# Kernel optimization log

Measured on AMD Instinct MI355X. Metric: run time of the kernel, lower is better.

The kernel has to match this reference:

```python
import jax, jax.numpy as jnp
import numpy as np

BATCH = 32768
HIDDEN = 512
OUT = 2
FUTURE_STEPS = 60


def _lstm_cell(x, h, c, w_ih, w_hh, b_ih, b_hh):
    # PyTorch gate order: i, f, g, o
    g = x @ w_ih.T + h @ w_hh.T + b_ih + b_hh
    i, f, gg, o = jnp.split(g, 4, axis=-1)
    c_new = jax.nn.sigmoid(f) * c + jax.nn.sigmoid(i) * jnp.tanh(gg)
    h_new = jax.nn.sigmoid(o) * jnp.tanh(c_new)
    return h_new, c_new


def setup_inputs() -> dict:
    key = jax.random.key(0)
    ks = jax.random.split(key, 16)
    s = 0.05
    inp = {
        "h": jax.random.normal(ks[0], (BATCH, HIDDEN), jnp.float32),
        "w_init_h": jax.random.normal(ks[1], (HIDDEN, HIDDEN), jnp.float32) * s,
        "b_init_h": jax.random.normal(ks[2], (HIDDEN,), jnp.float32) * s,
        "w_init_c": jax.random.normal(ks[3], (HIDDEN, HIDDEN), jnp.float32) * s,
        "b_init_c": jax.random.normal(ks[4], (HIDDEN,), jnp.float32) * s,
        "w_ih0": jax.random.normal(ks[5], (4 * HIDDEN, OUT), jnp.float32) * s,
        "w_hh0": jax.random.normal(ks[6], (4 * HIDDEN, HIDDEN), jnp.float32) * s,
        "b_ih0": jax.random.normal(ks[7], (4 * HIDDEN,), jnp.float32) * s,
        "b_hh0": jax.random.normal(ks[8], (4 * HIDDEN,), jnp.float32) * s,
        "w_ih1": jax.random.normal(ks[9], (4 * HIDDEN, HIDDEN), jnp.float32) * s,
        "w_hh1": jax.random.normal(ks[10], (4 * HIDDEN, HIDDEN), jnp.float32) * s,
        "b_ih1": jax.random.normal(ks[11], (4 * HIDDEN,), jnp.float32) * s,
        "b_hh1": jax.random.normal(ks[12], (4 * HIDDEN,), jnp.float32) * s,
        "w_out": jax.random.normal(ks[13], (OUT, HIDDEN), jnp.float32) * s,
        "b_out": jax.random.normal(ks[14], (OUT,), jnp.float32) * s,
    }
    return inp


def reference(h, w_init_h, b_init_h, w_init_c, b_init_c,
              w_ih0, w_hh0, b_ih0, b_hh0,
              w_ih1, w_hh1, b_ih1, b_hh1,
              w_out, b_out):
    batch = h.shape[0]
    # same initial (h, c) replicated to both LSTM layers (repeat(2,1,1))
    h0 = h @ w_init_h.T + b_init_h
    c0 = h @ w_init_c.T + b_init_c
    x0 = jnp.zeros((batch, OUT), h.dtype)

    def step(carry, _):
        x, h1, c1, h2, c2 = carry
        h1, c1 = _lstm_cell(x, h1, c1, w_ih0, w_hh0, b_ih0, b_hh0)
        h2, c2 = _lstm_cell(h1, h2, c2, w_ih1, w_hh1, b_ih1, b_hh1)
        pred = h2 @ w_out.T + b_out  # [batch, OUT]
        return (pred, h1, c1, h2, c2), pred

    _, preds = jax.lax.scan(step, (x0, h0, c0, h0, c0), None, length=FUTURE_STEPS)
    return jnp.transpose(preds, (1, 0, 2))  # [batch, future_steps, OUT]
```

## Files before the change

kernel.cpp:

```cpp
#include <hip/hip_runtime.h>

#define HID    512
#define TPB    512
#define NSTEP  60
#define BMI    64

using f32x4 = __attribute__((ext_vector_type(4))) float;
using s16x8 = __attribute__((ext_vector_type(8))) short;

__device__ __forceinline__ unsigned short f2bf(float f) {
    unsigned u = __builtin_bit_cast(unsigned, f);
    u += 0x7fffu + ((u >> 16) & 1u);
    return (unsigned short)(u >> 16);
}
__device__ __forceinline__ float bf2f(unsigned u) {
    return __builtin_bit_cast(float, u << 16);
}
__device__ __forceinline__ float sigm(float x) { return 1.0f / (1.0f + __expf(-x)); }
__device__ __forceinline__ float tanh_(float x) { return 1.0f - 2.0f / (__expf(2.0f * x) + 1.0f); }

__device__ __forceinline__ f32x4 deperm(f32x4 q, int lgr) {
    f32x4 p;
    if (lgr == 0)      { p[0]=q[0]; p[1]=q[1]; p[2]=q[2]; p[3]=q[3]; }
    else if (lgr == 1) { p[0]=q[1]; p[1]=q[0]; p[2]=q[3]; p[3]=q[2]; }
    else if (lgr == 2) { p[0]=q[2]; p[1]=q[3]; p[2]=q[0]; p[3]=q[1]; }
    else               { p[0]=q[3]; p[1]=q[2]; p[2]=q[1]; p[3]=q[0]; }
    return p;
}

__global__ void pack_kernel(const float* __restrict__ w_hh0, const float* __restrict__ w_ih1,
                            const float* __restrict__ w_hh1, const float* __restrict__ w_init_h,
                            const float* __restrict__ w_init_c,
                            const float* __restrict__ b_ih0, const float* __restrict__ b_hh0,
                            const float* __restrict__ b_ih1, const float* __restrict__ b_hh1,
                            unsigned short* __restrict__ PW1, unsigned short* __restrict__ PW2,
                            unsigned short* __restrict__ PI,
                            float* __restrict__ b1, float* __restrict__ b2)
{
    int idx = blockIdx.x * 256 + threadIdx.x;
    if (idx < 1048576) {
        int el = idx & 511, fr = idx >> 9;
        int ks = fr & 15, ct = (fr >> 4) & 7, s = fr >> 7;
        int lane = el >> 3, e = el & 7;
        int cl = ct * 16 + (lane & 15);
        int gcol = (cl >> 5) * 512 + s * 32 + (cl & 31);
        int k = ks * 32 + (lane >> 4) * 8 + e;
        PW1[idx] = f2bf(w_hh0[gcol * 512 + k]);
        return;
    }
    int i2 = idx - 1048576;
    if (i2 >= 0 && i2 < 2097152) {
        int el = i2 & 511, fr = i2 >> 9;
        int ks = fr & 31, ct = (fr >> 5) & 7, s = fr >> 8;
        int lane = el >> 3, e = el & 7;
        int cl = ct * 16 + (lane & 15);
        int gcol = (cl >> 5) * 512 + s * 32 + (cl & 31);
        int kk = (ks & 15) * 32 + (lane >> 4) * 8 + e;
        float v = (ks < 16) ? w_ih1[gcol * 512 + kk] : w_hh1[gcol * 512 + kk];
        PW2[i2] = f2bf(v);
        return;
    }
    int i3 = idx - (1048576 + 2097152);
    if (i3 >= 0 && i3 < 524288) {
        int el = i3 & 511, fr = i3 >> 9;
        int ks = fr & 15, tile = fr >> 4;
        int s = tile >> 5, c = tile & 31;
        int lane = el >> 3, e = el & 7;
        int n = c * 16 + (lane & 15);
        int k = ks * 32 + (lane >> 4) * 8 + e;
        float v = s ? w_init_c[n * 512 + k] : w_init_h[n * 512 + k];
        PI[i3] = f2bf(v);
        return;
    }
    int i4 = idx - (1048576 + 2097152 + 524288);
    if (i4 >= 0 && i4 < 2048) b1[i4] = b_ih0[i4] + b_hh0[i4];
    else if (i4 >= 2048 && i4 < 4096) b2[i4 - 2048] = b_ih1[i4 - 2048] + b_hh1[i4 - 2048];
}

__global__ __launch_bounds__(TPB, 2) void init_kernel(
    const float* __restrict__ hin, const unsigned short* __restrict__ PI,
    const float* __restrict__ b_init_h, const float* __restrict__ b_init_c,
    unsigned short* __restrict__ h1s, unsigned short* __restrict__ h2s,
    unsigned short* __restrict__ c1s, unsigned short* __restrict__ c2s)
{
    __shared__ unsigned short bufA[BMI * HID];
    const int tid = threadIdx.x, lane = tid & 63, wave = tid >> 6;
    const int m0 = blockIdx.x * BMI;
    const int l15 = lane & 15, lg = lane >> 4;
    const int swz = (lane & 7) << 4;

    for (int j = 0; j < 16; ++j) {
        int e = tid * 4 + j * 2048;
        int row = e >> 9, col = e & 511;
        float4 v = *(const float4*)(hin + (size_t)(m0 + row) * HID + col);
        ushort4 w;
        w.x = f2bf(v.x); w.y = f2bf(v.y); w.z = f2bf(v.z); w.w = f2bf(v.w);
        int L = (row * 1024 + col * 2) ^ ((row & 7) << 4);
        *(ushort4*)((char*)bufA + L) = w;
    }
    __syncthreads();

    #pragma unroll 1
    for (int cc = 0; cc < 4; ++cc) {
        int c = wave * 4 + cc;
        int nc = c * 16 + l15;
        f32x4 acc[4][2];
        #pragma unroll
        for (int rt = 0; rt < 4; ++rt)
            #pragma unroll
            for (int s = 0; s < 2; ++s)
                #pragma unroll
                for (int r = 0; r < 4; ++r) acc[rt][s][r] = 0.0f;

        #pragma unroll
        for (int ks = 0; ks < 16; ++ks) {
            s16x8 a[4];
            #pragma unroll
            for (int rt = 0; rt < 4; ++rt) {
                int ao = (rt * 16 + l15) * 1024 + ((ks * 64 + lg * 16) ^ swz);
                a[rt] = *(const s16x8*)((const char*)bufA + ao);
            }
            #pragma unroll
            for (int s = 0; s < 2; ++s) {
                s16x8 b = ((const s16x8*)PI)[((s * 32 + c) * 16 + ks) * 64 + lane];
                #pragma unroll
                for (int rt = 0; rt < 4; ++rt)
                    acc[rt][s] = __builtin_amdgcn_mfma_f32_16x16x32_bf16(a[rt], b, acc[rt][s], 0, 0, 0);
            }
        }
        float bh = b_init_h[nc], bc = b_init_c[nc];
        #pragma unroll
        for (int rt = 0; rt < 4; ++rt)
            #pragma unroll
            for (int r = 0; r < 4; ++r) {
                int m = m0 + rt * 16 + lg * 4 + r;
                float hv = acc[rt][0][r] + bh;
                float cv = acc[rt][1][r] + bc;
                unsigned short hb = f2bf(hv);
                size_t o = (size_t)m * HID + nc;
                h1s[o] = hb; h2s[o] = hb;
                c1s[o] = f2bf(cv); c2s[o] = f2bf(cv);
            }
    }
}

__global__ __launch_bounds__(TPB, 2) void l1_kernel(
    const unsigned short* __restrict__ h1R, unsigned short* __restrict__ h1W,
    unsigned short* __restrict__ c1s, const float* __restrict__ pp,
    float* __restrict__ outp, const unsigned short* __restrict__ PW1,
    const float* __restrict__ b1, const float* __restrict__ w_ih0,
    const float* __restrict__ b_out, int t)
{
    __shared__ __align__(16) unsigned short Ab[16384];
    __shared__ __align__(16) float gl[2][2][2048];
    __shared__ __align__(16) float xls[5120];

    const int tid = threadIdx.x, lane = tid & 63, w = tid >> 6;
    const int b = blockIdx.x;
    const int g = 2 * (b & 7) + (b >> 7);
    const int s = (b >> 3) & 15;
    const int m0 = g * 2048;
    const int l15 = lane & 15, lg = lane >> 4;
    const int cg = w & 1, kh = (w >> 1) & 1, rha = w >> 2;

    s16x8 bw[4][8];
    #pragma unroll
    for (int j = 0; j < 4; ++j)
        #pragma unroll
        for (int ksl = 0; ksl < 8; ++ksl)
            bw[j][ksl] = ((const s16x8*)PW1)[(((s * 8 + cg * 4 + j) * 16) + kh * 8 + ksl) * 64 + lane];

    const int erow = tid >> 4, ejp = tid & 15;
    const int lgr = w & 3;
    float b1v[8], wiA[8], wiB[8];
    #pragma unroll
    for (int q = 0; q < 8; ++q) {
        int dj = q & 1, gq = q >> 1;
        int gcol = gq * 512 + s * 32 + ejp * 2 + dj;
        b1v[q] = b1[gcol];
        wiA[q] = w_ih0[gcol * 2 + 0];
        wiB[q] = w_ih0[gcol * 2 + 1];
    }
    float bo0 = b_out[0], bo1 = b_out[1];

    if (t == 0) {
        #pragma unroll
        for (int i = 0; i < 8; ++i) xls[tid * 8 + i] = 0.0f;
    } else {
        f32x4 s0 = {0.f,0.f,0.f,0.f}, s1 = {0.f,0.f,0.f,0.f};
        #pragma unroll 1
        for (int ss = 0; ss < 16; ++ss) {
            const float* p = pp + (((size_t)(g * 16 + ss)) << 12) + tid * 8;
            s0 += *(const f32x4*)p;
            s1 += *(const f32x4*)(p + 4);
        }
        s0[0] += bo0; s0[1] += bo1; s0[2] += bo0; s0[3] += bo1;
        s1[0] += bo0; s1[1] += bo1; s1[2] += bo0; s1[3] += bo1;
        *(f32x4*)(xls + tid * 8) = s0;
        *(f32x4*)(xls + tid * 8 + 4) = s1;
        if (s == 0) {
            float* ob = outp + (size_t)(m0 + tid * 4) * (2 * NSTEP) + (t - 1) * 2;
            *(float2*)(ob)                 = make_float2(s0[0], s0[1]);
            *(float2*)(ob + 2 * NSTEP)     = make_float2(s0[2], s0[3]);
            *(float2*)(ob + 4 * NSTEP)     = make_float2(s1[0], s1[1]);
            *(float2*)(ob + 6 * NSTEP)     = make_float2(s1[2], s1[3]);
        }
    }

    const int sl15 = tid & 15, slg = (tid >> 4) & 3, srh = (tid >> 6) & 1, skq = tid >> 7;
    const int sgrow = srh * 16 + sl15;
    const int scol  = (tid & 15) * 0;
    (void)scol;

    uint4 nv[4];
    #pragma unroll
    for (int p = 0; p < 4; ++p) {
        int ks = p * 4 + skq;
        nv[p] = *(const uint4*)(h1R + (size_t)(m0 + sgrow) * HID + ks * 32 + slg * 8);
    }
    #pragma unroll
    for (int p = 0; p < 4; ++p)
        *(uint4*)((char*)Ab + p * 8192 + tid * 16) = nv[p];

    #pragma unroll 1
    for (int ch = 0; ch < 64; ++ch) {
        __syncthreads();

        if (ch < 63) {
            #pragma unroll
            for (int p = 0; p < 4; ++p) {
                int ks = p * 4 + skq;
                nv[p] = *(const uint4*)(h1R + (size_t)(m0 + (ch + 1) * 32 + sgrow) * HID + ks * 32 + slg * 8);
            }
        }

        f32x4 acc[4];
        #pragma unroll
        for (int j = 0; j < 4; ++j) { acc[j][0]=0.f; acc[j][1]=0.f; acc[j][2]=0.f; acc[j][3]=0.f; }
        #pragma unroll
        for (int ksl = 0; ksl < 8; ++ksl) {
            int ks = kh * 8 + ksl;
            s16x8 a = *(const s16x8*)((const char*)Ab + ks * 2048 + rha * 1024 + lane * 16);
            #pragma unroll
            for (int j = 0; j < 4; ++j)
                acc[j] = __builtin_amdgcn_mfma_f32_16x16x32_bf16(a, bw[j][ksl], acc[j], 0, 0, 0);
        }
        #pragma unroll
        for (int j = 0; j < 4; ++j) {
            int col = (cg * 4 + j) * 16 + l15;
            int u = col & 31, gate = col >> 5;
            float* dst = &gl[kh][u & 1][(u >> 1) * 4 + (gate ^ lg)];
            #pragma unroll
            for (int r = 0; r < 4; ++r)
                dst[(rha * 16 + lg * 4 + r) * 64] = acc[j][r];
        }
        __syncthreads();

        if (ch < 63) {
            #pragma unroll
            for (int p = 0; p < 4; ++p)
                *(uint4*)((char*)Ab + p * 8192 + tid * 16) = nv[p];
        }

        {
            int grow = ch * 32 + erow;
            int m = m0 + grow;
            float x0 = xls[grow * 2 + 0], x1 = xls[grow * 2 + 1];
            int gbase = erow * 64 + ejp * 4;
            f32x4 qa = *(const f32x4*)&gl[0][0][gbase];
            qa += *(const f32x4*)&gl[1][0][gbase];
            f32x4 qb = *(const f32x4*)&gl[0][1][gbase];
            qb += *(const f32x4*)&gl[1][1][gbase];
            qa = deperm(qa, lgr); qb = deperm(qb, lgr);

            int cix = m * HID + s * 32 + ejp * 2;
            unsigned cp = *(const unsigned*)(c1s + cix);
            float cold0 = bf2f(cp & 0xffffu), cold1 = bf2f(cp >> 16);
            float i0 = sigm(qa[0] + b1v[0] + x0 * wiA[0] + x1 * wiB[0]);
            float f0 = sigm(qa[1] + b1v[2] + x0 * wiA[2] + x1 * wiB[2]);
            float g0 = tanh_(qa[2] + b1v[4] + x0 * wiA[4] + x1 * wiB[4]);
            float o0 = sigm(qa[3] + b1v[6] + x0 * wiA[6] + x1 * wiB[6]);
            float cn0 = f0 * cold0 + i0 * g0;
            float hn0 = o0 * tanh_(cn0);
            float i1 = sigm(qb[0] + b1v[1] + x0 * wiA[1] + x1 * wiB[1]);
            float f1 = sigm(qb[1] + b1v[3] + x0 * wiA[3] + x1 * wiB[3]);
            float g1 = tanh_(qb[2] + b1v[5] + x0 * wiA[5] + x1 * wiB[5]);
            float o1 = sigm(qb[3] + b1v[7] + x0 * wiA[7] + x1 * wiB[7]);
            float cn1 = f1 * cold1 + i1 * g1;
            float hn1 = o1 * tanh_(cn1);
            *(unsigned*)(c1s + cix) = (unsigned)f2bf(cn0) | ((unsigned)f2bf(cn1) << 16);
            *(unsigned*)(h1W + cix) = (unsigned)f2bf(hn0) | ((unsigned)f2bf(hn1) << 16);
        }
    }
}

__global__ __launch_bounds__(TPB, 2) void l2_kernel(
    const unsigned short* __restrict__ h1C, const unsigned short* __restrict__ h2R,
    unsigned short* __restrict__ h2W, unsigned short* __restrict__ c2s,
    float* __restrict__ pp,
    const unsigned short* __restrict__ PW2, const float* __restrict__ b2,
    const float* __restrict__ w_out)
{
    __shared__ __align__(16) unsigned short Ab[32768];
    __shared__ __align__(16) float gl[2][2][2304];

    const int tid = threadIdx.x, lane = tid & 63, w = tid >> 6;
    const int b = blockIdx.x;
    const int g = 2 * (b & 7) + (b >> 7);
    const int s = (b >> 3) & 15;
    const int m0 = g * 2048;
    const int l15 = lane & 15, lg = lane >> 4;
    const int cg = w & 1, kq = w >> 1;
    const int copy = kq >> 1, adder = ((kq & 1) == 0);

    s16x8 bw[4][8];
    #pragma unroll
    for (int j = 0; j < 4; ++j)
        #pragma unroll
        for (int ksl = 0; ksl < 8; ++ksl)
            bw[j][ksl] = ((const s16x8*)PW2)[(((s * 8 + cg * 4 + j) * 32) + kq * 8 + ksl) * 64 + lane];

    const int erow = tid >> 4, ejp = tid & 15;
    const int lgr = w & 3;
    float b2v[8];
    #pragma unroll
    for (int q = 0; q < 8; ++q) {
        int dj = q & 1, gq = q >> 1;
        b2v[q] = b2[gq * 512 + s * 32 + ejp * 2 + dj];
    }
    float woA0 = w_out[s * 32 + ejp * 2], woA1 = w_out[s * 32 + ejp * 2 + 1];
    float woB0 = w_out[512 + s * 32 + ejp * 2], woB1 = w_out[512 + s * 32 + ejp * 2 + 1];

    const int sl15 = tid & 15, slg = (tid >> 4) & 3, srh = (tid >> 6) & 1, skq = tid >> 7;
    const int sgrow = srh * 16 + sl15;

    uint4 nv[8];
    #pragma unroll
    for (int p = 0; p < 8; ++p) {
        int ks = p * 4 + skq;
        const unsigned short* src = (p < 4) ? h1C : h2R;
        int kel = (p < 4) ? ks : (ks - 16);
        nv[p] = *(const uint4*)(src + (size_t)(m0 + sgrow) * HID + kel * 32 + slg * 8);
    }
    #pragma unroll
    for (int p = 0; p < 8; ++p)
        *(uint4*)((char*)Ab + p * 8192 + tid * 16) = nv[p];

    #pragma unroll 1
    for (int ch = 0; ch < 64; ++ch) {
        __syncthreads();

        if (ch < 63) {
            #pragma unroll
            for (int p = 0; p < 8; ++p) {
                int ks = p * 4 + skq;
                const unsigned short* src = (p < 4) ? h1C : h2R;
                int kel = (p < 4) ? ks : (ks - 16);
                nv[p] = *(const uint4*)(src + (size_t)(m0 + (ch + 1) * 32 + sgrow) * HID + kel * 32 + slg * 8);
            }
        }

        f32x4 acc[2][4];
        #pragma unroll
        for (int rh = 0; rh < 2; ++rh)
            #pragma unroll
            for (int j = 0; j < 4; ++j) { acc[rh][j][0]=0.f; acc[rh][j][1]=0.f; acc[rh][j][2]=0.f; acc[rh][j][3]=0.f; }
        #pragma unroll
        for (int ksl = 0; ksl < 8; ++ksl) {
            int ks = kq * 8 + ksl;
            s16x8 a0 = *(const s16x8*)((const char*)Ab + ks * 2048 + lane * 16);
            s16x8 a1 = *(const s16x8*)((const char*)Ab + ks * 2048 + 1024 + lane * 16);
            #pragma unroll
            for (int j = 0; j < 4; ++j) {
                acc[0][j] = __builtin_amdgcn_mfma_f32_16x16x32_bf16(a0, bw[j][ksl], acc[0][j], 0, 0, 0);
                acc[1][j] = __builtin_amdgcn_mfma_f32_16x16x32_bf16(a1, bw[j][ksl], acc[1][j], 0, 0, 0);
            }
        }

        if (!adder) {
            #pragma unroll
            for (int j = 0; j < 4; ++j) {
                int col = (cg * 4 + j) * 16 + l15;
                int u = col & 31, gate = col >> 5;
                float* dst = &gl[copy][u & 1][(u >> 1) * 4 + (gate ^ lg)];
                #pragma unroll
                for (int rh = 0; rh < 2; ++rh)
                    #pragma unroll
                    for (int r = 0; r < 4; ++r)
                        dst[(rh * 16 + lg * 4 + r) * 64] = acc[rh][j][r];
            }
        }
        __syncthreads();
        if (adder) {
            #pragma unroll
            for (int j = 0; j < 4; ++j) {
                int col = (cg * 4 + j) * 16 + l15;
                int u = col & 31, gate = col >> 5;
                float* dst = &gl[copy][u & 1][(u >> 1) * 4 + (gate ^ lg)];
                #pragma unroll
                for (int rh = 0; rh < 2; ++rh)
                    #pragma unroll
                    for (int r = 0; r < 4; ++r)
                        dst[(rh * 16 + lg * 4 + r) * 64] += acc[rh][j][r];
            }
        }
        __syncthreads();

        if (ch < 63) {
            #pragma unroll
            for (int p = 0; p < 8; ++p)
                *(uint4*)((char*)Ab + p * 8192 + tid * 16) = nv[p];
        }

        {
            int m = m0 + ch * 32 + erow;
            int gbase = erow * 64 + ejp * 4;
            f32x4 qa = *(const f32x4*)&gl[0][0][gbase];
            qa += *(const f32x4*)&gl[1][0][gbase];
            f32x4 qb = *(const f32x4*)&gl[0][1][gbase];
            qb += *(const f32x4*)&gl[1][1][gbase];
            qa = deperm(qa, lgr); qb = deperm(qb, lgr);

            int cix = m * HID + s * 32 + ejp * 2;
            unsigned cp = *(const unsigned*)(c2s + cix);
            float cold0 = bf2f(cp & 0xffffu), cold1 = bf2f(cp >> 16);
            float i0 = sigm(qa[0] + b2v[0]);
            float f0 = sigm(qa[1] + b2v[2]);
            float g0 = tanh_(qa[2] + b2v[4]);
            float o0 = sigm(qa[3] + b2v[6]);
            float cn0 = f0 * cold0 + i0 * g0;
            float hn0 = o0 * tanh_(cn0);
            float i1 = sigm(qb[0] + b2v[1]);
            float f1 = sigm(qb[1] + b2v[3]);
            float g1 = tanh_(qb[2] + b2v[5]);
            float o1 = sigm(qb[3] + b2v[7]);
            float cn1 = f1 * cold1 + i1 * g1;
            float hn1 = o1 * tanh_(cn1);
            *(unsigned*)(c2s + cix) = (unsigned)f2bf(cn0) | ((unsigned)f2bf(cn1) << 16);
            *(unsigned*)(h2W + cix) = (unsigned)f2bf(hn0) | ((unsigned)f2bf(hn1) << 16);

            float p0 = hn0 * woA0 + hn1 * woA1;
            float p1 = hn0 * woB0 + hn1 * woB1;
            #pragma unroll
            for (int d = 1; d < 16; d <<= 1) {
                p0 += __shfl_xor(p0, d, 16);
                p1 += __shfl_xor(p1, d, 16);
            }
            if (ejp == 0)
                *(float2*)(pp + (((size_t)(g * 16 + s)) << 12) + (size_t)(ch * 32 + erow) * 2)
                    = make_float2(p0, p1);
        }
    }
}

__global__ void tail_kernel(const float* __restrict__ pp, const float* __restrict__ b_out,
                            float* __restrict__ outp)
{
    int i = blockIdx.x * 256 + threadIdx.x;
    if (i < 65536) {
        int m = i >> 1, j = i & 1;
        int g = m >> 11;
        int idx = (m & 2047) * 2 + j;
        float sum = b_out[j];
        #pragma unroll 1
        for (int s = 0; s < 16; ++s)
            sum += pp[(((size_t)(g * 16 + s)) << 12) + idx];
        outp[(size_t)m * (2 * NSTEP) + (NSTEP - 1) * 2 + j] = sum;
    }
}

extern "C" void kernel_launch(void* const* d_in, const int* in_sizes, int n_in,
                              void* d_out, int out_size, void* d_ws, size_t ws_size,
                              hipStream_t stream)
{
    (void)in_sizes; (void)n_in; (void)out_size; (void)ws_size;
    const float* h        = (const float*)d_in[0];
    const float* w_init_h = (const float*)d_in[1];
    const float* b_init_h = (const float*)d_in[2];
    const float* w_init_c = (const float*)d_in[3];
    const float* b_init_c = (const float*)d_in[4];
    const float* w_ih0    = (const float*)d_in[5];
    const float* w_hh0    = (const float*)d_in[6];
    const float* b_ih0    = (const float*)d_in[7];
    const float* b_hh0    = (const float*)d_in[8];
    const float* w_ih1    = (const float*)d_in[9];
    const float* w_hh1    = (const float*)d_in[10];
    const float* b_ih1    = (const float*)d_in[11];
    const float* b_hh1    = (const float*)d_in[12];
    const float* w_out    = (const float*)d_in[13];
    const float* b_out    = (const float*)d_in[14];
    float* out = (float*)d_out;

    char* ws = (char*)d_ws;
    unsigned short* h1s[2] = { (unsigned short*)(ws + 0),
                               (unsigned short*)(ws + 33554432) };
    unsigned short* h2s[2] = { (unsigned short*)(ws + 67108864),
                               (unsigned short*)(ws + 100663296) };
    unsigned short* c1s = (unsigned short*)(ws + 134217728);
    unsigned short* c2s = (unsigned short*)(ws + 167772160);
    float* pp           = (float*)(ws + 201326592);
    unsigned short* PW1 = (unsigned short*)(ws + 205520896);
    unsigned short* PW2 = (unsigned short*)(ws + 207618048);
    unsigned short* PI  = (unsigned short*)(ws + 211812352);
    float* b1 = (float*)(ws + 212860928);
    float* b2 = (float*)(ws + 212869120);

    pack_kernel<<<14352, 256, 0, stream>>>(w_hh0, w_ih1, w_hh1, w_init_h, w_init_c,
                                           b_ih0, b_hh0, b_ih1, b_hh1, PW1, PW2, PI, b1, b2);
    init_kernel<<<32768 / BMI, TPB, 0, stream>>>(h, PI, b_init_h, b_init_c,
                                                 h1s[1], h2s[1], c1s, c2s);
    for (int t = 0; t < NSTEP; ++t) {
        const unsigned short* h1R = h1s[(t + 1) & 1];
        unsigned short* h1W = h1s[t & 1];
        const unsigned short* h2R = h2s[(t + 1) & 1];
        unsigned short* h2W = h2s[t & 1];
        l1_kernel<<<256, TPB, 0, stream>>>(h1R, h1W, c1s, pp, out, PW1, b1, w_ih0, b_out, t);
        l2_kernel<<<256, TPB, 0, stream>>>(h1W, h2R, h2W, c2s, pp, PW2, b2, w_out);
    }
    tail_kernel<<<256, 256, 0, stream>>>(pp, b_out, out);
}
```

Measured before the change: 38.76 ms.

## Halve l1 tile rows, double grid, and use LDS atomics for k-split reductions

l1_kernel now processes 16-row chunks over 1024-row groups, launches 512 blocks with launch bounds for 4 blocks per CU, and halves the B-fragment registers and LDS footprint to raise occupancy. Both kernels replace the separate per-k-half gate buffers and two-phase adder scheme with LDS float atomicAdd into a single zeroed buffer, which the epilogue reads and clears. The old-cell-state load is hoisted ahead of the MFMA loop to overlap its latency. LDS atomics may serialise, and the smaller l1 tile halves weight reuse per loaded A row.

```diff
diff --git a/kernel.cpp b/kernel.cpp
--- a/kernel.cpp
+++ b/kernel.cpp
@@ -144,82 +144,72 @@
     }
 }
 
-__global__ __launch_bounds__(TPB, 2) void l1_kernel(
+__global__ __launch_bounds__(512, 4) void l1_kernel(
     const unsigned short* __restrict__ h1R, unsigned short* __restrict__ h1W,
     unsigned short* __restrict__ c1s, const float* __restrict__ pp,
     float* __restrict__ outp, const unsigned short* __restrict__ PW1,
     const float* __restrict__ b1, const float* __restrict__ w_ih0,
     const float* __restrict__ b_out, int t)
 {
-    __shared__ __align__(16) unsigned short Ab[16384];
-    __shared__ __align__(16) float gl[2][2][2048];
-    __shared__ __align__(16) float xls[5120];
+    __shared__ __align__(16) unsigned short Ab[8192];
+    __shared__ __align__(16) float gl[2][1028];
+    __shared__ __align__(16) float xls[2048];
 
     const int tid = threadIdx.x, lane = tid & 63, w = tid >> 6;
     const int b = blockIdx.x;
-    const int g = 2 * (b & 7) + (b >> 7);
+    const int g = (b & 7) * 4 + (b >> 7);
     const int s = (b >> 3) & 15;
-    const int m0 = g * 2048;
+    const int m0 = g * 1024;
     const int l15 = lane & 15, lg = lane >> 4;
-    const int cg = w & 1, kh = (w >> 1) & 1, rha = w >> 2;
-
-    s16x8 bw[4][8];
-    #pragma unroll
-    for (int j = 0; j < 4; ++j)
+    const int cg = w >> 1, kh = w & 1;
+
+    for (int i = tid; i < 2056; i += 512) ((float*)gl)[i] = 0.f;
+
+    s16x8 bw[2][8];
+    #pragma unroll
+    for (int j = 0; j < 2; ++j)
         #pragma unroll
         for (int ksl = 0; ksl < 8; ++ksl)
-            bw[j][ksl] = ((const s16x8*)PW1)[(((s * 8 + cg * 4 + j) * 16) + kh * 8 + ksl) * 64 + lane];
-
-    const int erow = tid >> 4, ejp = tid & 15;
-    const int lgr = w & 3;
-    float b1v[8], wiA[8], wiB[8];
-    #pragma unroll
-    for (int q = 0; q < 8; ++q) {
-        int dj = q & 1, gq = q >> 1;
-        int gcol = gq * 512 + s * 32 + ejp * 2 + dj;
+            bw[j][ksl] = ((const s16x8*)PW1)[(((s * 8 + cg * 2 + j) * 16) + kh * 8 + ksl) * 64 + lane];
+
+    const int erow = tid >> 5, eu = tid & 31;
+    const int lgr = erow >> 2;
+    float b1v[4], wiA[4], wiB[4];
+    #pragma unroll
+    for (int q = 0; q < 4; ++q) {
+        int gcol = q * 512 + s * 32 + eu;
         b1v[q] = b1[gcol];
         wiA[q] = w_ih0[gcol * 2 + 0];
         wiB[q] = w_ih0[gcol * 2 + 1];
     }
-    float bo0 = b_out[0], bo1 = b_out[1];
+    const float bo0 = b_out[0], bo1 = b_out[1];
 
     if (t == 0) {
         #pragma unroll
-        for (int i = 0; i < 8; ++i) xls[tid * 8 + i] = 0.0f;
+        for (int i = 0; i < 4; ++i) xls[tid * 4 + i] = 0.0f;
     } else {
-        f32x4 s0 = {0.f,0.f,0.f,0.f}, s1 = {0.f,0.f,0.f,0.f};
+        f32x4 s0 = {0.f, 0.f, 0.f, 0.f};
         #pragma unroll 1
-        for (int ss = 0; ss < 16; ++ss) {
-            const float* p = pp + (((size_t)(g * 16 + ss)) << 12) + tid * 8;
-            s0 += *(const f32x4*)p;
-            s1 += *(const f32x4*)(p + 4);
-        }
+        for (int ss = 0; ss < 16; ++ss)
+            s0 += *(const f32x4*)(pp + (((size_t)((g >> 1) * 16 + ss)) << 12)
+                                  + (g & 1) * 2048 + tid * 4);
         s0[0] += bo0; s0[1] += bo1; s0[2] += bo0; s0[3] += bo1;
-        s1[0] += bo0; s1[1] += bo1; s1[2] += bo0; s1[3] += bo1;
-        *(f32x4*)(xls + tid * 8) = s0;
-        *(f32x4*)(xls + tid * 8 + 4) = s1;
+        *(f32x4*)(xls + tid * 4) = s0;
         if (s == 0) {
-            float* ob = outp + (size_t)(m0 + tid * 4) * (2 * NSTEP) + (t - 1) * 2;
-            *(float2*)(ob)                 = make_float2(s0[0], s0[1]);
-            *(float2*)(ob + 2 * NSTEP)     = make_float2(s0[2], s0[3]);
-            *(float2*)(ob + 4 * NSTEP)     = make_float2(s1[0], s1[1]);
-            *(float2*)(ob + 6 * NSTEP)     = make_float2(s1[2], s1[3]);
-        }
-    }
-
-    const int sl15 = tid & 15, slg = (tid >> 4) & 3, srh = (tid >> 6) & 1, skq = tid >> 7;
-    const int sgrow = srh * 16 + sl15;
-    const int scol  = (tid & 15) * 0;
-    (void)scol;
-
-    uint4 nv[4];
-    #pragma unroll
-    for (int p = 0; p < 4; ++p) {
-        int ks = p * 4 + skq;
-        nv[p] = *(const uint4*)(h1R + (size_t)(m0 + sgrow) * HID + ks * 32 + slg * 8);
-    }
-    #pragma unroll
-    for (int p = 0; p < 4; ++p)
+            float* ob = outp + (size_t)(m0 + tid * 2) * (2 * NSTEP) + (t - 1) * 2;
+            *(float2*)(ob)             = make_float2(s0[0], s0[1]);
+            *(float2*)(ob + 2 * NSTEP) = make_float2(s0[2], s0[3]);
+        }
+    }
+
+    const int st_row = tid & 15, st_lg = (tid >> 4) & 3, st_ks = tid >> 6;
+
+    uint4 nv[2];
+    #pragma unroll
+    for (int p = 0; p < 2; ++p)
+        nv[p] = *(const uint4*)(h1R + (size_t)(m0 + st_row) * HID + (p * 8 + st_ks) * 32 + st_lg * 8);
+    #pragma unroll
+    for (int p = 0; p < 2; ++p)
         *(uint4*)((char*)Ab + p * 8192 + tid * 16) = nv[p];
 
     #pragma unroll 1
@@ -228,73 +218,60 @@
 
         if (ch < 63) {
             #pragma unroll
-            for (int p = 0; p < 4; ++p) {
-                int ks = p * 4 + skq;
-                nv[p] = *(const uint4*)(h1R + (size_t)(m0 + (ch + 1) * 32 + sgrow) * HID + ks * 32 + slg * 8);
-            }
-        }
-
-        f32x4 acc[4];
-        #pragma unroll
-        for (int j = 0; j < 4; ++j) { acc[j][0]=0.f; acc[j][1]=0.f; acc[j][2]=0.f; acc[j][3]=0.f; }
+            for (int p = 0; p < 2; ++p)
+                nv[p] = *(const uint4*)(h1R + (size_t)(m0 + (ch + 1) * 16 + st_row) * HID
+                                        + (p * 8 + st_ks) * 32 + st_lg * 8);
+        }
+        unsigned short cw = c1s[(size_t)(m0 + ch * 16 + erow) * HID + s * 32 + eu];
+
+        f32x4 acc[2];
+        #pragma unroll
+        for (int j = 0; j < 2; ++j) { acc[j][0]=0.f; acc[j][1]=0.f; acc[j][2]=0.f; acc[j][3]=0.f; }
         #pragma unroll
         for (int ksl = 0; ksl < 8; ++ksl) {
-            int ks = kh * 8 + ksl;
-            s16x8 a = *(const s16x8*)((const char*)Ab + ks * 2048 + rha * 1024 + lane * 16);
-            #pragma unroll
-            for (int j = 0; j < 4; ++j)
+            s16x8 a = *(const s16x8*)((const char*)Ab + (kh * 8 + ksl) * 1024 + lane * 16);
+            #pragma unroll
+            for (int j = 0; j < 2; ++j)
                 acc[j] = __builtin_amdgcn_mfma_f32_16x16x32_bf16(a, bw[j][ksl], acc[j], 0, 0, 0);
         }
         #pragma unroll
-        for (int j = 0; j < 4; ++j) {
-            int col = (cg * 4 + j) * 16 + l15;
+        for (int j = 0; j < 2; ++j) {
+            int col = (cg * 2 + j) * 16 + l15;
             int u = col & 31, gate = col >> 5;
-            float* dst = &gl[kh][u & 1][(u >> 1) * 4 + (gate ^ lg)];
             #pragma unroll
             for (int r = 0; r < 4; ++r)
-                dst[(rha * 16 + lg * 4 + r) * 64] = acc[j][r];
+                atomicAdd(&gl[u & 1][(lg * 4 + r) * 64 + (u >> 1) * 4 + (gate ^ lg)], acc[j][r]);
         }
         __syncthreads();
 
         if (ch < 63) {
             #pragma unroll
-            for (int p = 0; p < 4; ++p)
+            for (int p = 0; p < 2; ++p)
                 *(uint4*)((char*)Ab + p * 8192 + tid * 16) = nv[p];
         }
 
         {
-            int grow = ch * 32 + erow;
-            int m = m0 + grow;
-            float x0 = xls[grow * 2 + 0], x1 = xls[grow * 2 + 1];
-            int gbase = erow * 64 + ejp * 4;
-            f32x4 qa = *(const f32x4*)&gl[0][0][gbase];
-            qa += *(const f32x4*)&gl[1][0][gbase];
-            f32x4 qb = *(const f32x4*)&gl[0][1][gbase];
-            qb += *(const f32x4*)&gl[1][1][gbase];
-            qa = deperm(qa, lgr); qb = deperm(qb, lgr);
-
-            int cix = m * HID + s * 32 + ejp * 2;
-            unsigned cp = *(const unsigned*)(c1s + cix);
-            float cold0 = bf2f(cp & 0xffffu), cold1 = bf2f(cp >> 16);
-            float i0 = sigm(qa[0] + b1v[0] + x0 * wiA[0] + x1 * wiB[0]);
-            float f0 = sigm(qa[1] + b1v[2] + x0 * wiA[2] + x1 * wiB[2]);
-            float g0 = tanh_(qa[2] + b1v[4] + x0 * wiA[4] + x1 * wiB[4]);
-            float o0 = sigm(qa[3] + b1v[6] + x0 * wiA[6] + x1 * wiB[6]);
-            float cn0 = f0 * cold0 + i0 * g0;
-            float hn0 = o0 * tanh_(cn0);
-            float i1 = sigm(qb[0] + b1v[1] + x0 * wiA[1] + x1 * wiB[1]);
-            float f1 = sigm(qb[1] + b1v[3] + x0 * wiA[3] + x1 * wiB[3]);
-            float g1 = tanh_(qb[2] + b1v[5] + x0 * wiA[5] + x1 * wiB[5]);
-            float o1 = sigm(qb[3] + b1v[7] + x0 * wiA[7] + x1 * wiB[7]);
-            float cn1 = f1 * cold1 + i1 * g1;
-            float hn1 = o1 * tanh_(cn1);
-            *(unsigned*)(c1s + cix) = (unsigned)f2bf(cn0) | ((unsigned)f2bf(cn1) << 16);
-            *(unsigned*)(h1W + cix) = (unsigned)f2bf(hn0) | ((unsigned)f2bf(hn1) << 16);
-        }
-    }
-}
-
-__global__ __launch_bounds__(TPB, 2) void l2_kernel(
+            int mloc = ch * 16 + erow;
+            float x0 = xls[mloc * 2 + 0], x1 = xls[mloc * 2 + 1];
+            float* gp = &gl[eu & 1][erow * 64 + (eu >> 1) * 4];
+            f32x4 q = *(const f32x4*)gp;
+            *(f32x4*)gp = (f32x4){0.f, 0.f, 0.f, 0.f};
+            q = deperm(q, lgr);
+            float iv = sigm(q[0] + b1v[0] + x0 * wiA[0] + x1 * wiB[0]);
+            float fv = sigm(q[1] + b1v[1] + x0 * wiA[1] + x1 * wiB[1]);
+            float gv = tanh_(q[2] + b1v[2] + x0 * wiA[2] + x1 * wiB[2]);
+            float ov = sigm(q[3] + b1v[3] + x0 * wiA[3] + x1 * wiB[3]);
+            float cold = bf2f(cw);
+            float cn = fv * cold + iv * gv;
+            float hn = ov * tanh_(cn);
+            size_t cix = (size_t)(m0 + mloc) * HID + s * 32 + eu;
+            c1s[cix] = f2bf(cn);
+            h1W[cix] = f2bf(hn);
+        }
+    }
+}
+
+__global__ __launch_bounds__(512, 2) void l2_kernel(
     const unsigned short* __restrict__ h1C, const unsigned short* __restrict__ h2R,
     unsigned short* __restrict__ h2W, unsigned short* __restrict__ c2s,
     float* __restrict__ pp,
@@ -302,7 +279,7 @@
     const float* __restrict__ w_out)
 {
     __shared__ __align__(16) unsigned short Ab[32768];
-    __shared__ __align__(16) float gl[2][2][2304];
+    __shared__ __align__(16) float gl[2][2052];
 
     const int tid = threadIdx.x, lane = tid & 63, w = tid >> 6;
     const int b = blockIdx.x;
@@ -311,7 +288,8 @@
     const int m0 = g * 2048;
     const int l15 = lane & 15, lg = lane >> 4;
     const int cg = w & 1, kq = w >> 1;
-    const int copy = kq >> 1, adder = ((kq & 1) == 0);
+
+    for (int i = tid; i < 4104; i += 512) ((float*)gl)[i] = 0.f;
 
     s16x8 bw[4][8];
     #pragma unroll
@@ -331,16 +309,16 @@
     float woA0 = w_out[s * 32 + ejp * 2], woA1 = w_out[s * 32 + ejp * 2 + 1];
     float woB0 = w_out[512 + s * 32 + ejp * 2], woB1 = w_out[512 + s * 32 + ejp * 2 + 1];
 
-    const int sl15 = tid & 15, slg = (tid >> 4) & 3, srh = (tid >> 6) & 1, skq = tid >> 7;
-    const int sgrow = srh * 16 + sl15;
+    const int st_l15 = tid & 15, st_lg = (tid >> 4) & 3, st_rh = (tid >> 6) & 1, st_ks = tid >> 7;
+    const int st_row = st_rh * 16 + st_l15;
 
     uint4 nv[8];
     #pragma unroll
     for (int p = 0; p < 8; ++p) {
-        int ks = p * 4 + skq;
-        const unsigned short* src = (p < 4) ? h1C : h2R;
-        int kel = (p < 4) ? ks : (ks - 16);
-        nv[p] = *(const uint4*)(src + (size_t)(m0 + sgrow) * HID + kel * 32 + slg * 8);
+        int ks = p * 4 + st_ks;
+        const unsigned short* src = (ks < 16) ? h1C : h2R;
+        int kel = (ks < 16) ? ks : (ks - 16);
+        nv[p] = *(const uint4*)(src + (size_t)(m0 + st_row) * HID + kel * 32 + st_lg * 8);
     }
     #pragma unroll
     for (int p = 0; p < 8; ++p)
@@ -353,12 +331,13 @@
         if (ch < 63) {
             #pragma unroll
             for (int p = 0; p < 8; ++p) {
-                int ks = p * 4 + skq;
-                const unsigned short* src = (p < 4) ? h1C : h2R;
-                int kel = (p < 4) ? ks : (ks - 16);
-                nv[p] = *(const uint4*)(src + (size_t)(m0 + (ch + 1) * 32 + sgrow) * HID + kel * 32 + slg * 8);
-            }
-        }
+                int ks = p * 4 + st_ks;
+                const unsigned short* src = (ks < 16) ? h1C : h2R;
+                int kel = (ks < 16) ? ks : (ks - 16);
+                nv[p] = *(const uint4*)(src + (size_t)(m0 + (ch + 1) * 32 + st_row) * HID + kel * 32 + st_lg * 8);
+            }
+        }
+        unsigned cw = *(const unsigned*)(c2s + (size_t)(m0 + ch * 32 + erow) * HID + s * 32 + ejp * 2);
 
         f32x4 acc[2][4];
         #pragma unroll
@@ -376,33 +355,16 @@
                 acc[1][j] = __builtin_amdgcn_mfma_f32_16x16x32_bf16(a1, bw[j][ksl], acc[1][j], 0, 0, 0);
             }
         }
-
-        if (!adder) {
-            #pragma unroll
-            for (int j = 0; j < 4; ++j) {
-                int col = (cg * 4 + j) * 16 + l15;
-                int u = col & 31, gate = col >> 5;
-                float* dst = &gl[copy][u & 1][(u >> 1) * 4 + (gate ^ lg)];
+        #pragma unroll
+        for (int j = 0; j < 4; ++j) {
+            int col = (cg * 4 + j) * 16 + l15;
+            int u = col & 31, gate = col >> 5;
+            #pragma unroll
+            for (int rh = 0; rh < 2; ++rh)
                 #pragma unroll
-                for (int rh = 0; rh < 2; ++rh)
-                    #pragma unroll
-                    for (int r = 0; r < 4; ++r)
-                        dst[(rh * 16 + lg * 4 + r) * 64] = acc[rh][j][r];
-            }
-        }
-        __syncthreads();
-        if (adder) {
-            #pragma unroll
-            for (int j = 0; j < 4; ++j) {
-                int col = (cg * 4 + j) * 16 + l15;
-                int u = col & 31, gate = col >> 5;
-                float* dst = &gl[copy][u & 1][(u >> 1) * 4 + (gate ^ lg)];
-                #pragma unroll
-                for (int rh = 0; rh < 2; ++rh)
-                    #pragma unroll
-                    for (int r = 0; r < 4; ++r)
-                        dst[(rh * 16 + lg * 4 + r) * 64] += acc[rh][j][r];
-            }
+                for (int r = 0; r < 4; ++r)
+                    atomicAdd(&gl[u & 1][(rh * 16 + lg * 4 + r) * 64 + (u >> 1) * 4 + (gate ^ lg)],
+                              acc[rh][j][r]);
         }
         __syncthreads();
 
@@ -413,17 +375,17 @@
         }
 
         {
-            int m = m0 + ch * 32 + erow;
+            int mloc = ch * 32 + erow;
             int gbase = erow * 64 + ejp * 4;
-            f32x4 qa = *(const f32x4*)&gl[0][0][gbase];
-            qa += *(const f32x4*)&gl[1][0][gbase];
-            f32x4 qb = *(const f32x4*)&gl[0][1][gbase];
-            qb += *(const f32x4*)&gl[1][1][gbase];
+            float* gpa = &gl[0][gbase];
+            float* gpb = &gl[1][gbase];
+            f32x4 qa = *(const f32x4*)gpa;
+            f32x4 qb = *(const f32x4*)gpb;
+            *(f32x4*)gpa = (f32x4){0.f, 0.f, 0.f, 0.f};
+            *(f32x4*)gpb = (f32x4){0.f, 0.f, 0.f, 0.f};
             qa = deperm(qa, lgr); qb = deperm(qb, lgr);
 
-            int cix = m * HID + s * 32 + ejp * 2;
-            unsigned cp = *(const unsigned*)(c2s + cix);
-            float cold0 = bf2f(cp & 0xffffu), cold1 = bf2f(cp >> 16);
+            float cold0 = bf2f(cw & 0xffffu), cold1 = bf2f(cw >> 16);
             float i0 = sigm(qa[0] + b2v[0]);
             float f0 = sigm(qa[1] + b2v[2]);
             float g0 = tanh_(qa[2] + b2v[4]);
@@ -436,6 +398,7 @@
             float o1 = sigm(qb[3] + b2v[7]);
             float cn1 = f1 * cold1 + i1 * g1;
             float hn1 = o1 * tanh_(cn1);
+            size_t cix = (size_t)(m0 + mloc) * HID + s * 32 + ejp * 2;
             *(unsigned*)(c2s + cix) = (unsigned)f2bf(cn0) | ((unsigned)f2bf(cn1) << 16);
             *(unsigned*)(h2W + cix) = (unsigned)f2bf(hn0) | ((unsigned)f2bf(hn1) << 16);
 
@@ -447,7 +410,7 @@
                 p1 += __shfl_xor(p1, d, 16);
             }
             if (ejp == 0)
-                *(float2*)(pp + (((size_t)(g * 16 + s)) << 12) + (size_t)(ch * 32 + erow) * 2)
+                *(float2*)(pp + (((size_t)(g * 16 + s)) << 12) + (size_t)mloc * 2)
                     = make_float2(p0, p1);
         }
     }
@@ -514,8 +477,8 @@
         unsigned short* h1W = h1s[t & 1];
         const unsigned short* h2R = h2s[(t + 1) & 1];
         unsigned short* h2W = h2s[t & 1];
-        l1_kernel<<<256, TPB, 0, stream>>>(h1R, h1W, c1s, pp, out, PW1, b1, w_ih0, b_out, t);
-        l2_kernel<<<256, TPB, 0, stream>>>(h1W, h2R, h2W, c2s, pp, PW2, b2, w_out);
+        l1_kernel<<<512, 512, 0, stream>>>(h1R, h1W, c1s, pp, out, PW1, b1, w_ih0, b_out, t);
+        l2_kernel<<<256, 512, 0, stream>>>(h1W, h2R, h2W, c2s, pp, PW2, b2, w_out);
     }
     tail_kernel<<<256, 256, 0, stream>>>(pp, b_out, out);
 }
```

Result: slower. 146.7 ms (+278.5%).

## Tile hidden-state buffers by column slice and double-prefetch A chunks two ahead

Applied to the files above, without the earlier changes.

Changes the h/c state storage from row-major [batch][512] to a blocked layout [group][slice][2048 rows][32 cols], so each block's writes and each A-tile load read contiguous 64-byte segments. The A-operand prefetch now runs two chunks ahead with a second register buffer, and the cell-state load is issued early in the loop instead of in the epilogue. The goal is better memory coalescing and more latency hiding for global loads. The cost is higher register pressure from doubling the prefetch registers, which matters most in l2 (16 uint4 per thread), and could reduce occupancy or cause spills.

```diff
diff --git a/kernel.cpp b/kernel.cpp
--- a/kernel.cpp
+++ b/kernel.cpp
@@ -129,15 +129,17 @@
             }
         }
         float bh = b_init_h[nc], bc = b_init_c[nc];
+        int sl = nc >> 5, ul = nc & 31;
         #pragma unroll
         for (int rt = 0; rt < 4; ++rt)
             #pragma unroll
             for (int r = 0; r < 4; ++r) {
                 int m = m0 + rt * 16 + lg * 4 + r;
+                int gg = m >> 11, lr = m & 2047;
                 float hv = acc[rt][0][r] + bh;
                 float cv = acc[rt][1][r] + bc;
                 unsigned short hb = f2bf(hv);
-                size_t o = (size_t)m * HID + nc;
+                size_t o = ((size_t)(gg * 16 + sl) * 2048 + lr) * 32 + ul;
                 h1s[o] = hb; h2s[o] = hb;
                 c1s[o] = f2bf(cv); c2s[o] = f2bf(cv);
             }
@@ -153,15 +155,16 @@
 {
     __shared__ __align__(16) unsigned short Ab[16384];
     __shared__ __align__(16) float gl[2][2][2048];
-    __shared__ __align__(16) float xls[5120];
+    __shared__ __align__(16) float xls[4160];
 
     const int tid = threadIdx.x, lane = tid & 63, w = tid >> 6;
     const int b = blockIdx.x;
     const int g = 2 * (b & 7) + (b >> 7);
     const int s = (b >> 3) & 15;
-    const int m0 = g * 2048;
     const int l15 = lane & 15, lg = lane >> 4;
     const int cg = w & 1, kh = (w >> 1) & 1, rha = w >> 2;
+    const size_t gB = (size_t)g * 16;
+    const size_t blkOff = (gB + s) * 2048 * 32;
 
     s16x8 bw[4][8];
     #pragma unroll
@@ -199,40 +202,40 @@
         *(f32x4*)(xls + tid * 8) = s0;
         *(f32x4*)(xls + tid * 8 + 4) = s1;
         if (s == 0) {
-            float* ob = outp + (size_t)(m0 + tid * 4) * (2 * NSTEP) + (t - 1) * 2;
-            *(float2*)(ob)                 = make_float2(s0[0], s0[1]);
-            *(float2*)(ob + 2 * NSTEP)     = make_float2(s0[2], s0[3]);
-            *(float2*)(ob + 4 * NSTEP)     = make_float2(s1[0], s1[1]);
-            *(float2*)(ob + 6 * NSTEP)     = make_float2(s1[2], s1[3]);
-        }
-    }
-
-    const int sl15 = tid & 15, slg = (tid >> 4) & 3, srh = (tid >> 6) & 1, skq = tid >> 7;
-    const int sgrow = srh * 16 + sl15;
-    const int scol  = (tid & 15) * 0;
-    (void)scol;
-
-    uint4 nv[4];
-    #pragma unroll
-    for (int p = 0; p < 4; ++p) {
-        int ks = p * 4 + skq;
-        nv[p] = *(const uint4*)(h1R + (size_t)(m0 + sgrow) * HID + ks * 32 + slg * 8);
-    }
+            float* ob = outp + (size_t)(g * 2048 + tid * 4) * (2 * NSTEP) + (t - 1) * 2;
+            *(float2*)(ob)             = make_float2(s0[0], s0[1]);
+            *(float2*)(ob + 2 * NSTEP) = make_float2(s0[2], s0[3]);
+            *(float2*)(ob + 4 * NSTEP) = make_float2(s1[0], s1[1]);
+            *(float2*)(ob + 6 * NSTEP) = make_float2(s1[2], s1[3]);
+        }
+    }
+
+    const int st_ks4 = tid >> 7;
+    const int st_row = ((tid >> 6) & 1) * 16 + (tid & 15);
+    const int st_lg  = (tid >> 4) & 3;
+
+    uint4 nvW[4], nvF[4];
     #pragma unroll
     for (int p = 0; p < 4; ++p)
-        *(uint4*)((char*)Ab + p * 8192 + tid * 16) = nv[p];
+        nvF[p] = *(const uint4*)(h1R + ((gB + (p * 4 + st_ks4)) * 2048 + st_row) * 32 + st_lg * 8);
+    #pragma unroll
+    for (int p = 0; p < 4; ++p)
+        *(uint4*)((char*)Ab + p * 8192 + tid * 16) = nvF[p];
+    #pragma unroll
+    for (int p = 0; p < 4; ++p)
+        nvW[p] = *(const uint4*)(h1R + ((gB + (p * 4 + st_ks4)) * 2048 + 32 + st_row) * 32 + st_lg * 8);
 
     #pragma unroll 1
     for (int ch = 0; ch < 64; ++ch) {
         __syncthreads();
 
-        if (ch < 63) {
-            #pragma unroll
-            for (int p = 0; p < 4; ++p) {
-                int ks = p * 4 + skq;
-                nv[p] = *(const uint4*)(h1R + (size_t)(m0 + (ch + 1) * 32 + sgrow) * HID + ks * 32 + slg * 8);
-            }
-        }
+        if (ch < 62) {
+            #pragma unroll
+            for (int p = 0; p < 4; ++p)
+                nvF[p] = *(const uint4*)(h1R + ((gB + (p * 4 + st_ks4)) * 2048
+                                         + (ch + 2) * 32 + st_row) * 32 + st_lg * 8);
+        }
+        unsigned cw = *(const unsigned*)(c1s + blkOff + (size_t)(ch * 32 + erow) * 32 + ejp * 2);
 
         f32x4 acc[4];
         #pragma unroll
@@ -259,13 +262,14 @@
         if (ch < 63) {
             #pragma unroll
             for (int p = 0; p < 4; ++p)
-                *(uint4*)((char*)Ab + p * 8192 + tid * 16) = nv[p];
+                *(uint4*)((char*)Ab + p * 8192 + tid * 16) = nvW[p];
+            #pragma unroll
+            for (int p = 0; p < 4; ++p) nvW[p] = nvF[p];
         }
 
         {
-            int grow = ch * 32 + erow;
-            int m = m0 + grow;
-            float x0 = xls[grow * 2 + 0], x1 = xls[grow * 2 + 1];
+            int mloc = ch * 32 + erow;
+            float x0 = xls[mloc * 2 + 0], x1 = xls[mloc * 2 + 1];
             int gbase = erow * 64 + ejp * 4;
             f32x4 qa = *(const f32x4*)&gl[0][0][gbase];
             qa += *(const f32x4*)&gl[1][0][gbase];
@@ -273,9 +277,7 @@
             qb += *(const f32x4*)&gl[1][1][gbase];
             qa = deperm(qa, lgr); qb = deperm(qb, lgr);
 
-            int cix = m * HID + s * 32 + ejp * 2;
-            unsigned cp = *(const unsigned*)(c1s + cix);
-            float cold0 = bf2f(cp & 0xffffu), cold1 = bf2f(cp >> 16);
+            float cold0 = bf2f(cw & 0xffffu), cold1 = bf2f(cw >> 16);
             float i0 = sigm(qa[0] + b1v[0] + x0 * wiA[0] + x1 * wiB[0]);
             float f0 = sigm(qa[1] + b1v[2] + x0 * wiA[2] + x1 * wiB[2]);
             float g0 = tanh_(qa[2] + b1v[4] + x0 * wiA[4] + x1 * wiB[4]);
@@ -288,6 +290,7 @@
             float o1 = sigm(qb[3] + b1v[7] + x0 * wiA[7] + x1 * wiB[7]);
             float cn1 = f1 * cold1 + i1 * g1;
             float hn1 = o1 * tanh_(cn1);
+            size_t cix = blkOff + (size_t)mloc * 32 + ejp * 2;
             *(unsigned*)(c1s + cix) = (unsigned)f2bf(cn0) | ((unsigned)f2bf(cn1) << 16);
             *(unsigned*)(h1W + cix) = (unsigned)f2bf(hn0) | ((unsigned)f2bf(hn1) << 16);
         }
@@ -308,10 +311,11 @@
     const int b = blockIdx.x;
     const int g = 2 * (b & 7) + (b >> 7);
     const int s = (b >> 3) & 15;
-    const int m0 = g * 2048;
     const int l15 = lane & 15, lg = lane >> 4;
     const int cg = w & 1, kq = w >> 1;
     const int copy = kq >> 1, adder = ((kq & 1) == 0);
+    const size_t gB = (size_t)g * 16;
+    const size_t blkOff = (gB + s) * 2048 * 32;
 
     s16x8 bw[4][8];
     #pragma unroll
@@ -331,34 +335,43 @@
     float woA0 = w_out[s * 32 + ejp * 2], woA1 = w_out[s * 32 + ejp * 2 + 1];
     float woB0 = w_out[512 + s * 32 + ejp * 2], woB1 = w_out[512 + s * 32 + ejp * 2 + 1];
 
-    const int sl15 = tid & 15, slg = (tid >> 4) & 3, srh = (tid >> 6) & 1, skq = tid >> 7;
-    const int sgrow = srh * 16 + sl15;
-
-    uint4 nv[8];
+    const int st_ks4 = tid >> 7;
+    const int st_row = ((tid >> 6) & 1) * 16 + (tid & 15);
+    const int st_lg  = (tid >> 4) & 3;
+
+    uint4 nvW[8], nvF[8];
     #pragma unroll
     for (int p = 0; p < 8; ++p) {
-        int ks = p * 4 + skq;
-        const unsigned short* src = (p < 4) ? h1C : h2R;
-        int kel = (p < 4) ? ks : (ks - 16);
-        nv[p] = *(const uint4*)(src + (size_t)(m0 + sgrow) * HID + kel * 32 + slg * 8);
+        int ks = p * 4 + st_ks4;
+        const unsigned short* base = (ks < 16) ? h1C : h2R;
+        int ksl = (ks < 16) ? ks : (ks - 16);
+        nvF[p] = *(const uint4*)(base + ((gB + ksl) * 2048 + st_row) * 32 + st_lg * 8);
     }
     #pragma unroll
     for (int p = 0; p < 8; ++p)
-        *(uint4*)((char*)Ab + p * 8192 + tid * 16) = nv[p];
+        *(uint4*)((char*)Ab + p * 8192 + tid * 16) = nvF[p];
+    #pragma unroll
+    for (int p = 0; p < 8; ++p) {
+        int ks = p * 4 + st_ks4;
+        const unsigned short* base = (ks < 16) ? h1C : h2R;
+        int ksl = (ks < 16) ? ks : (ks - 16);
+        nvW[p] = *(const uint4*)(base + ((gB + ksl) * 2048 + 32 + st_row) * 32 + st_lg * 8);
+    }
 
     #pragma unroll 1
     for (int ch = 0; ch < 64; ++ch) {
         __syncthreads();
 
-        if (ch < 63) {
+        if (ch < 62) {
             #pragma unroll
             for (int p = 0; p < 8; ++p) {
-                int ks = p * 4 + skq;
-                const unsigned short* src = (p < 4) ? h1C : h2R;
-                int kel = (p < 4) ? ks : (ks - 16);
-                nv[p] = *(const uint4*)(src + (size_t)(m0 + (ch + 1) * 32 + sgrow) * HID + kel * 32 + slg * 8);
-            }
-        }
+                int ks = p * 4 + st_ks4;
+                const unsigned short* base = (ks < 16) ? h1C : h2R;
+                int ksl = (ks < 16) ? ks : (ks - 16);
+                nvF[p] = *(const uint4*)(base + ((gB + ksl) * 2048 + (ch + 2) * 32 + st_row) * 32 + st_lg * 8);
+            }
+        }
+        unsigned cw = *(const unsigned*)(c2s + blkOff + (size_t)(ch * 32 + erow) * 32 + ejp * 2);
 
         f32x4 acc[2][4];
         #pragma unroll
@@ -409,11 +422,13 @@
         if (ch < 63) {
             #pragma unroll
             for (int p = 0; p < 8; ++p)
-                *(uint4*)((char*)Ab + p * 8192 + tid * 16) = nv[p];
+                *(uint4*)((char*)Ab + p * 8192 + tid * 16) = nvW[p];
+            #pragma unroll
+            for (int p = 0; p < 8; ++p) nvW[p] = nvF[p];
         }
 
         {
-            int m = m0 + ch * 32 + erow;
+            int mloc = ch * 32 + erow;
             int gbase = erow * 64 + ejp * 4;
             f32x4 qa = *(const f32x4*)&gl[0][0][gbase];
             qa += *(const f32x4*)&gl[1][0][gbase];
@@ -421,9 +436,7 @@
             qb += *(const f32x4*)&gl[1][1][gbase];
             qa = deperm(qa, lgr); qb = deperm(qb, lgr);
 
-            int cix = m * HID + s * 32 + ejp * 2;
-            unsigned cp = *(const unsigned*)(c2s + cix);
-            float cold0 = bf2f(cp & 0xffffu), cold1 = bf2f(cp >> 16);
+            float cold0 = bf2f(cw & 0xffffu), cold1 = bf2f(cw >> 16);
             float i0 = sigm(qa[0] + b2v[0]);
             float f0 = sigm(qa[1] + b2v[2]);
             float g0 = tanh_(qa[2] + b2v[4]);
@@ -436,6 +449,7 @@
             float o1 = sigm(qb[3] + b2v[7]);
             float cn1 = f1 * cold1 + i1 * g1;
             float hn1 = o1 * tanh_(cn1);
+            size_t cix = blkOff + (size_t)mloc * 32 + ejp * 2;
             *(unsigned*)(c2s + cix) = (unsigned)f2bf(cn0) | ((unsigned)f2bf(cn1) << 16);
             *(unsigned*)(h2W + cix) = (unsigned)f2bf(hn0) | ((unsigned)f2bf(hn1) << 16);
 
@@ -447,7 +461,7 @@
                 p1 += __shfl_xor(p1, d, 16);
             }
             if (ejp == 0)
-                *(float2*)(pp + (((size_t)(g * 16 + s)) << 12) + (size_t)(ch * 32 + erow) * 2)
+                *(float2*)(pp + (((size_t)(g * 16 + s)) << 12) + (size_t)mloc * 2)
                     = make_float2(p0, p1);
         }
     }
@@ -514,8 +528,8 @@
         unsigned short* h1W = h1s[t & 1];
         const unsigned short* h2R = h2s[(t + 1) & 1];
         unsigned short* h2W = h2s[t & 1];
-        l1_kernel<<<256, TPB, 0, stream>>>(h1R, h1W, c1s, pp, out, PW1, b1, w_ih0, b_out, t);
-        l2_kernel<<<256, TPB, 0, stream>>>(h1W, h2R, h2W, c2s, pp, PW2, b2, w_out);
+        l1_kernel<<<256, 512, 0, stream>>>(h1R, h1W, c1s, pp, out, PW1, b1, w_ih0, b_out, t);
+        l2_kernel<<<256, 512, 0, stream>>>(h1W, h2R, h2W, c2s, pp, PW2, b2, w_out);
     }
     tail_kernel<<<256, 256, 0, stream>>>(pp, b_out, out);
 }
```

Result: slower. 58.96 ms (+52.1%).
